# Optimization experiments

Measured on AMD Instinct MI355X. Metric: run time of the kernel, lower is better.

## Reference

```python
import jax, jax.numpy as jnp
import numpy as np

B, T, C, H = 2, 2048, 1024, 16
DH = C // H
EPS = 1e-5


def _rotary(t_len, d_head):
    inv_freq = 1.0 / (10000.0 ** (jnp.arange(0, d_head, 2, dtype=jnp.float32) / d_head))
    t = jnp.arange(t_len, dtype=jnp.float32)
    freqs = t[:, None] * inv_freq[None, :]           # [T, dh/2]
    emb = jnp.concatenate([freqs, freqs], axis=-1)    # [T, dh]
    return jnp.cos(emb), jnp.sin(emb)


def _apply_rope(x, cos, sin):
    # x: [B,H,T,dh]; cos/sin: [T,dh]
    d = x.shape[-1]
    x1, x2 = x[..., : d // 2], x[..., d // 2 :]
    x_rot = jnp.concatenate([-x2, x1], axis=-1)
    return x * cos + x_rot * sin


def _decay_mask(t_len, n_head):
    gammas = 1.0 - 2.0 ** (-5.0 - jnp.arange(n_head, dtype=jnp.float32))  # [H]
    n = jnp.arange(t_len)[:, None]
    m = jnp.arange(t_len)[None, :]
    dist = n - m
    decay = gammas[:, None, None] ** jnp.maximum(dist, 0).astype(jnp.float32)
    return jnp.where(dist[None] >= 0, decay, 0.0)  # [H,T,T]


def setup_inputs() -> dict:
    key = jax.random.key(0)
    ks = jax.random.split(key, 7)
    s = 1.0 / np.sqrt(C)
    return {
        "x": jax.random.normal(ks[0], (B, T, C), dtype=jnp.float32),
        "Wq": jax.random.normal(ks[1], (C, C), dtype=jnp.float32) * s,
        "Wk": jax.random.normal(ks[2], (C, C), dtype=jnp.float32) * s,
        "Wv": jax.random.normal(ks[3], (C, C), dtype=jnp.float32) * s,
        "Wo": jax.random.normal(ks[4], (C, C), dtype=jnp.float32) * s,
        "gn_weight": jnp.ones((C,), dtype=jnp.float32),
        "gn_bias": jnp.zeros((C,), dtype=jnp.float32),
    }


def reference(x, Wq, Wk, Wv, Wo, gn_weight, gn_bias):
    b, t, c = x.shape
    # projections (torch Linear: y = x @ W.T), split heads -> [B,H,T,dh]
    def proj(W):
        return jnp.einsum("btc,oc->bto", x, W).reshape(b, t, H, DH).transpose(0, 2, 1, 3)
    q, k, v = proj(Wq), proj(Wk), proj(Wv)

    cos, sin = _rotary(t, DH)
    q = _apply_rope(q, cos, sin)
    k = _apply_rope(k, cos, sin)

    decay = _decay_mask(t, H)                          # [H,T,T]
    qk = jnp.einsum("bhtd,bhsd->bhts", q, k) * (1.0 / np.sqrt(DH))
    qk = qk * decay[None]
    out = jnp.einsum("bhts,bhsd->bhtd", qk, v)         # [B,H,T,dh]

    # GroupNorm with n_head groups over channels, per token
    out = out.transpose(0, 2, 1, 3)                    # [B,T,H,dh]
    mu = jnp.mean(out, axis=-1, keepdims=True)
    var = jnp.mean((out - mu) ** 2, axis=-1, keepdims=True)
    out = (out - mu) * jax.lax.rsqrt(var + EPS)
    out = out * gn_weight.reshape(H, DH) + gn_bias.reshape(H, DH)

    out = out.reshape(b, t, c)
    return jnp.einsum("btc,oc->bto", out, Wo)
```

## Files before the change

kernel.cpp:

```cpp
#include <hip/hip_runtime.h>
#include <stdint.h>

#define B_ 2
#define T_ 2048
#define C_ 1024
#define H_ 16
#define DH_ 64
#define M_ (B_*T_)

typedef short bhalf8 __attribute__((ext_vector_type(8)));
typedef float floatx4 __attribute__((ext_vector_type(4)));

__device__ __forceinline__ short f2bf(float f) {
  unsigned u = __float_as_uint(f);
  u += 0x7fffu + ((u >> 16) & 1u);
  return (short)(u >> 16);
}

__device__ __forceinline__ void gll16(void* lds_dst, const void* g_src) {
  __builtin_amdgcn_global_load_lds(
      reinterpret_cast<const uint32_t __attribute__((address_space(1)))*>(
          reinterpret_cast<uintptr_t>(g_src)),
      reinterpret_cast<uint32_t __attribute__((address_space(3)))*>(
          reinterpret_cast<uintptr_t>(lds_dst)),
      16, 0, 0);
}

__global__ void cvt_all(
    const float* __restrict__ x,  const float* __restrict__ wq,
    const float* __restrict__ wk, const float* __restrict__ wv,
    const float* __restrict__ wo,
    short* __restrict__ xb, short* __restrict__ wqb, short* __restrict__ wkb,
    short* __restrict__ wvb, short* __restrict__ wob)
{
  int i = blockIdx.x * blockDim.x + threadIdx.x;
  const float* s; short* d; int off;
  if (i < (M_*C_/4)) { s = x; d = xb; off = i; }
  else {
    int j = i - M_*C_/4;
    int w = j >> 18;
    off = j & ((1<<18) - 1);
    s = (w==0) ? wq : (w==1) ? wk : (w==2) ? wv : wo;
    d = (w==0) ? wqb : (w==1) ? wkb : (w==2) ? wvb : wob;
  }
  float4 v = ((const float4*)s)[off];
  short4 o;
  o.x = f2bf(v.x); o.y = f2bf(v.y); o.z = f2bf(v.z); o.w = f2bf(v.w);
  ((short4*)d)[off] = o;
}

__global__ __launch_bounds__(256) void gemm_qkv(
    const short* __restrict__ X,
    const short* __restrict__ Wq, const short* __restrict__ Wk, const short* __restrict__ Wv,
    short* __restrict__ Qb, short* __restrict__ Kb, short* __restrict__ Vt)
{
  __shared__ __align__(16) short As[128*32];
  __shared__ __align__(16) short Bs[128*32];
  const int tid  = threadIdx.x;
  const int lane = tid & 63;
  const int wv   = tid >> 6;
  const int l15  = lane & 15;
  const int quad = lane >> 4;
  const int wm   = (wv >> 1) << 6;
  const int wn   = (wv & 1) << 6;
  const int nx   = blockIdx.x;
  const int m0   = blockIdx.y << 7;
  const int K    = C_;

  const short *Ab, *Bb;
  int nloc, kind;
  if (nx < 8)       { kind = 0; nloc = nx << 7;        Ab = X  + (size_t)m0*K;   Bb = Wq + (size_t)nloc*K; }
  else if (nx < 16) { kind = 1; nloc = (nx - 8) << 7;  Ab = X  + (size_t)m0*K;   Bb = Wk + (size_t)nloc*K; }
  else              { kind = 2; nloc = (nx - 16) << 7; Ab = Wv + (size_t)nloc*K; Bb = X  + (size_t)m0*K;   }

  floatx4 acc[4][4] = {};

  for (int k0 = 0; k0 < K; k0 += 32) {
    __syncthreads();
#pragma unroll
    for (int i = 0; i < 2; ++i) {
      int c = i*256 + tid;
      int row = c >> 2, off = (c & 3) * 8;
      gll16(&As[(i*256 + (wv<<6))*8], Ab + (size_t)row*K + k0 + off);
      gll16(&Bs[(i*256 + (wv<<6))*8], Bb + (size_t)row*K + k0 + off);
    }
    __syncthreads();
    bhalf8 af[4], bfr[4];
#pragma unroll
    for (int rt = 0; rt < 4; ++rt)
      af[rt] = *(const bhalf8*)&As[(wm + rt*16 + l15)*32 + quad*8];
#pragma unroll
    for (int ct = 0; ct < 4; ++ct)
      bfr[ct] = *(const bhalf8*)&Bs[(wn + ct*16 + l15)*32 + quad*8];
#pragma unroll
    for (int rt = 0; rt < 4; ++rt)
#pragma unroll
      for (int ct = 0; ct < 4; ++ct)
        acc[rt][ct] = __builtin_amdgcn_mfma_f32_16x16x32_bf16(af[rt], bfr[ct], acc[rt][ct], 0, 0, 0);
  }

  if (kind < 2) {
    short* Cb = kind ? Kb : Qb;
    const int hh = (nloc + wn) >> 6;
#pragma unroll
    for (int rt = 0; rt < 4; ++rt)
#pragma unroll
      for (int r = 0; r < 4; ++r) {
        int n  = m0 + wm + rt*16 + quad*4 + r;
        int bb = n >> 11, t = n & (T_-1);
        size_t base = ((size_t)(bb*H_ + hh)*T_ + t)*DH_;
        float tf = (float)t;
#pragma unroll
        for (int ct = 0; ct < 2; ++ct) {
          int ii = ct*16 + l15;
          float ang = tf * exp2f((float)ii * (-0.4152410118609203f));
          float sn = __sinf(ang), cs = __cosf(ang);
          float xlo = acc[rt][ct][r], xhi = acc[rt][ct+2][r];
          Cb[base + ii]      = f2bf(xlo*cs - xhi*sn);
          Cb[base + ii + 32] = f2bf(xhi*cs + xlo*sn);
        }
      }
  } else {
#pragma unroll
    for (int rt = 0; rt < 4; ++rt)
#pragma unroll
      for (int r = 0; r < 4; ++r) {
        int o = nloc + wm + rt*16 + quad*4 + r;
#pragma unroll
        for (int ct = 0; ct < 4; ++ct) {
          int n  = m0 + wn + ct*16 + l15;
          int bb = n >> 11, t = n & (T_-1);
          Vt[(size_t)bb*(C_*T_) + (size_t)o*T_ + t] = f2bf(acc[rt][ct][r]);
        }
      }
  }
}

__global__ __launch_bounds__(256) void gemm_out(
    const short* __restrict__ A, const short* __restrict__ Bm, float* __restrict__ Cf)
{
  __shared__ __align__(16) short As[128*64];
  __shared__ __align__(16) short Bs[64*64];
  const int tid = threadIdx.x, lane = tid & 63, wv = tid >> 6;
  const int l15 = lane & 15, quad = lane >> 4;
  const int n0 = blockIdx.x << 6;
  const int m0 = blockIdx.y << 7;

  floatx4 acc[2][4] = {};
  const short* Ab = A  + (size_t)m0 * C_;
  const short* Bb = Bm + (size_t)n0 * C_;

  for (int k0 = 0; k0 < C_; k0 += 64) {
    __syncthreads();
#pragma unroll
    for (int i = 0; i < 4; ++i) {
      int c = (i<<8) + tid, r = c >> 3, g = (c & 7) ^ (r & 7);
      gll16(&As[((i<<8) + (wv<<6))*8], Ab + (size_t)r*C_ + k0 + (g<<3));
    }
#pragma unroll
    for (int i = 0; i < 2; ++i) {
      int c = (i<<8) + tid, r = c >> 3, g = (c & 7) ^ (r & 7);
      gll16(&Bs[((i<<8) + (wv<<6))*8], Bb + (size_t)r*C_ + k0 + (g<<3));
    }
    __syncthreads();
#pragma unroll
    for (int ks = 0; ks < 2; ++ks) {
      bhalf8 af[2], bfr[4];
#pragma unroll
      for (int rt = 0; rt < 2; ++rt) {
        int row = (wv<<5) + rt*16 + l15;
        af[rt] = *(const bhalf8*)&As[(row<<6) + ((((ks<<2)+quad) ^ (row&7))<<3)];
      }
#pragma unroll
      for (int ct = 0; ct < 4; ++ct) {
        int row = ct*16 + l15;
        bfr[ct] = *(const bhalf8*)&Bs[(row<<6) + ((((ks<<2)+quad) ^ (row&7))<<3)];
      }
#pragma unroll
      for (int rt = 0; rt < 2; ++rt)
#pragma unroll
        for (int ct = 0; ct < 4; ++ct)
          acc[rt][ct] = __builtin_amdgcn_mfma_f32_16x16x32_bf16(af[rt], bfr[ct], acc[rt][ct], 0, 0, 0);
    }
  }

#pragma unroll
  for (int rt = 0; rt < 2; ++rt)
#pragma unroll
    for (int r = 0; r < 4; ++r) {
      int n = m0 + (wv<<5) + rt*16 + quad*4 + r;
#pragma unroll
      for (int ct = 0; ct < 4; ++ct)
        Cf[(size_t)n * C_ + n0 + ct*16 + l15] = acc[rt][ct][r];
    }
}

__global__ __launch_bounds__(256, 4) void retention(
    const short* __restrict__ Qb, const short* __restrict__ Kb, const short* __restrict__ Vt,
    const float* __restrict__ gnw, const float* __restrict__ gnb,
    short* __restrict__ Xn)
{
  __shared__ __align__(16) short Ks[2][64*64];
  __shared__ __align__(16) short Vs[2][64*64];
  __shared__ __align__(16) short Ss[64*64];

  const int tid = threadIdx.x, lane = tid & 63, wv = tid >> 6;
  const int l15 = lane & 15, quad = lane >> 4;

  const int flat = blockIdx.x;
  const int bh = (flat & 7) | (((flat >> 8) & 3) << 3);
  const int si = (flat >> 3) & 31;
  const int s  = (si & 1) ? (31 - (si >> 1)) : (si >> 1);
  const int b = bh >> 4, h = bh & 15;
  const int n0 = s << 6;

  const float log2g = log2f(1.f - exp2f(-5.f - (float)h));

  const short* Qg  = Qb + ((size_t)(b*H_ + h)*T_ + n0 + (wv<<4)) * DH_;
  const short* Kg  = Kb + ((size_t)(b*H_ + h)*T_) * DH_;
  const short* Vtg = Vt + (size_t)b*(C_*T_) + (size_t)h*DH_*T_;

  bhalf8 aq[2];
#pragma unroll
  for (int ks = 0; ks < 2; ++ks)
    aq[ks] = *(const bhalf8*)(Qg + (size_t)l15*DH_ + ks*32 + quad*8);

  float rowf[4], colf0[4];
#pragma unroll
  for (int r = 0; r < 4; ++r)
    rowf[r] = exp2f(log2g * (float)((wv<<4) + (quad<<2) + r)) * 0.125f;
#pragma unroll
  for (int ct = 0; ct < 4; ++ct)
    colf0[ct] = exp2f(-log2g * (float)(ct*16 + l15));

  int mt0 = 0;
  while (log2g * (float)(n0 - (mt0 << 6) - 63) < -34.f) ++mt0;
  const int mtmax = s;

  auto stage = [&](int buf, int mt) {
    const int m0s = mt << 6;
#pragma unroll
    for (int i = 0; i < 2; ++i) {
      int slot = (i<<8) + tid;
      int r = slot >> 3, g = (slot & 7) ^ (r & 7);
      gll16(&Ks[buf][((i<<8) + (wv<<6))*8], Kg  + (size_t)(m0s + r)*DH_ + (g<<3));
      gll16(&Vs[buf][((i<<8) + (wv<<6))*8], Vtg + (size_t)r*T_ + m0s + (g<<3));
    }
  };

  floatx4 oacc[4] = {};
  stage(0, mt0);
  int cur = 0;
  for (int mt = mt0; mt <= mtmax; ++mt, cur ^= 1) {
    const int m0 = mt << 6;
    __syncthreads();
    if (mt < mtmax) stage(cur ^ 1, mt + 1);

    floatx4 sacc[4] = {};
#pragma unroll
    for (int ks = 0; ks < 2; ++ks) {
      bhalf8 bk[4];
#pragma unroll
      for (int ct = 0; ct < 4; ++ct) {
        int row = ct*16 + l15;
        bk[ct] = *(const bhalf8*)&Ks[cur][(row<<6) + ((((ks<<2)+quad) ^ (row&7))<<3)];
      }
#pragma unroll
      for (int ct = 0; ct < 4; ++ct)
        sacc[ct] = __builtin_amdgcn_mfma_f32_16x16x32_bf16(aq[ks], bk[ct], sacc[ct], 0, 0, 0);
    }

    const float tilef = exp2f(log2g * (float)(n0 - m0));
    if (mt == mtmax) {
#pragma unroll
      for (int ct = 0; ct < 4; ++ct) {
        float cf = colf0[ct] * tilef;
        int colg = (ct<<1) + (l15>>3);
        int m = m0 + ct*16 + l15;
#pragma unroll
        for (int r = 0; r < 4; ++r) {
          int row = (wv<<4) + (quad<<2) + r;
          float v = (n0 + row >= m) ? sacc[ct][r] * (rowf[r] * cf) : 0.f;
          Ss[(row<<6) + ((colg ^ ((row>>1)&7))<<3) + (l15&7)] = f2bf(v);
        }
      }
    } else {
#pragma unroll
      for (int ct = 0; ct < 4; ++ct) {
        float cf = colf0[ct] * tilef;
        int colg = (ct<<1) + (l15>>3);
#pragma unroll
        for (int r = 0; r < 4; ++r) {
          int row = (wv<<4) + (quad<<2) + r;
          Ss[(row<<6) + ((colg ^ ((row>>1)&7))<<3) + (l15&7)] = f2bf(sacc[ct][r] * (rowf[r] * cf));
        }
      }
    }

#pragma unroll
    for (int ks = 0; ks < 2; ++ks) {
      int row = (wv<<4) + l15;
      bhalf8 as_ = *(const bhalf8*)&Ss[(row<<6) + ((((ks<<2)+quad) ^ ((row>>1)&7))<<3)];
      bhalf8 bv[4];
#pragma unroll
      for (int ct = 0; ct < 4; ++ct) {
        int vrow = ct*16 + l15;
        bv[ct] = *(const bhalf8*)&Vs[cur][(vrow<<6) + ((((ks<<2)+quad) ^ (vrow&7))<<3)];
      }
#pragma unroll
      for (int ct = 0; ct < 4; ++ct)
        oacc[ct] = __builtin_amdgcn_mfma_f32_16x16x32_bf16(as_, bv[ct], oacc[ct], 0, 0, 0);
    }
  }

#pragma unroll
  for (int r = 0; r < 4; ++r) {
    float s1 = oacc[0][r] + oacc[1][r] + oacc[2][r] + oacc[3][r];
    float s2 = oacc[0][r]*oacc[0][r] + oacc[1][r]*oacc[1][r]
             + oacc[2][r]*oacc[2][r] + oacc[3][r]*oacc[3][r];
#pragma unroll
    for (int off = 1; off < 16; off <<= 1) {
      s1 += __shfl_xor(s1, off);
      s2 += __shfl_xor(s2, off);
    }
    float mean = s1 * (1.f/64.f);
    float var  = s2 * (1.f/64.f) - mean*mean;
    float rstd = rsqrtf(var + 1e-5f);
    int t = n0 + (wv<<4) + (quad<<2) + r;
    size_t obase = ((size_t)b*T_ + t)*C_ + h*DH_;
#pragma unroll
    for (int ct = 0; ct < 4; ++ct) {
      int d = ct*16 + l15;
      float y = (oacc[ct][r] - mean)*rstd*gnw[h*DH_ + d] + gnb[h*DH_ + d];
      Xn[obase + d] = f2bf(y);
    }
  }
}

extern "C" void kernel_launch(void* const* d_in, const int* in_sizes, int n_in,
                              void* d_out, int out_size, void* d_ws, size_t ws_size,
                              hipStream_t stream) {
  (void)in_sizes; (void)n_in; (void)out_size; (void)ws_size;
  const float* x   = (const float*)d_in[0];
  const float* Wq  = (const float*)d_in[1];
  const float* Wk  = (const float*)d_in[2];
  const float* Wv  = (const float*)d_in[3];
  const float* Wo  = (const float*)d_in[4];
  const float* gnw = (const float*)d_in[5];
  const float* gnb = (const float*)d_in[6];
  float* out = (float*)d_out;

  char* ws = (char*)d_ws;
  short* Xb  = (short*)(ws);
  short* Wqb = (short*)(ws + (8u<<20));
  short* Wkb = (short*)(ws + (10u<<20));
  short* Wvb = (short*)(ws + (12u<<20));
  short* Wob = (short*)(ws + (14u<<20));
  short* Qb  = (short*)(ws + (16u<<20));
  short* Kb  = (short*)(ws + (24u<<20));
  short* Vtw = (short*)(ws + (32u<<20));
  short* Xn  = (short*)(ws + (40u<<20));

  cvt_all<<<(M_*C_/4 + 4*(C_*C_/4)) / 256, 256, 0, stream>>>(
      x, Wq, Wk, Wv, Wo, Xb, Wqb, Wkb, Wvb, Wob);

  gemm_qkv<<<dim3(24, 32), 256, 0, stream>>>(Xb, Wqb, Wkb, Wvb, Qb, Kb, Vtw);
  retention<<<1024, 256, 0, stream>>>(Qb, Kb, Vtw, gnw, gnb, Xn);
  gemm_out<<<dim3(16, 32), 256, 0, stream>>>(Xn, Wob, out);
}
```

Baseline: 204.4 us.

## Replace quadratic retention with chunkwise recurrent state formulation

Replaces the parallel retention kernel, which loops over all earlier key tiles, with a chunkwise formulation. A transposed K is built, per-segment KV states over groups of 8 chunks are precomputed, and each 64-token chunk combines an intra-chunk quadratic part with the decayed inter-chunk state. The state is stored as split hi/lo bf16 pairs to limit precision loss. This adds two extra kernel launches and aliases workspace buffers that earlier kernels used (Xb, Wqb). It also loops over up to 7 prior chunks inside each block.

```diff
diff --git a/kernel.cpp b/kernel.cpp
--- a/kernel.cpp
+++ b/kernel.cpp
@@ -15,6 +15,9 @@
   unsigned u = __float_as_uint(f);
   u += 0x7fffu + ((u >> 16) & 1u);
   return (short)(u >> 16);
+}
+__device__ __forceinline__ float bf2f(short s) {
+  return __uint_as_float(((unsigned)(unsigned short)s) << 16);
 }
 
 __device__ __forceinline__ void gll16(void* lds_dst, const void* g_src) {
@@ -195,30 +198,130 @@
     }
 }
 
-__global__ __launch_bounds__(256, 4) void retention(
-    const short* __restrict__ Qb, const short* __restrict__ Kb, const short* __restrict__ Vt,
+__global__ __launch_bounds__(256) void transpose_k(
+    const short* __restrict__ Kb, short* __restrict__ Kt)
+{
+  __shared__ short tile[64*66];
+  const int idx = blockIdx.x, bh = idx >> 5, tc = idx & 31;
+  const int t0 = tc << 6;
+  const short* src = Kb + ((size_t)bh*T_ + t0) * DH_;
+  int row = threadIdx.x >> 2, c0 = (threadIdx.x & 3) << 4;
+  *(int4*)&tile[row*66 + c0]     = *(const int4*)&src[row*64 + c0];
+  *(int4*)&tile[row*66 + c0 + 8] = *(const int4*)&src[row*64 + c0 + 8];
+  __syncthreads();
+  short* dst = Kt + (size_t)bh*DH_*T_;
+  int d = threadIdx.x >> 2, k0 = (threadIdx.x & 3) << 4;
+  short tmp[16];
+#pragma unroll
+  for (int i = 0; i < 16; ++i) tmp[i] = tile[(k0 + i)*66 + d];
+  *(int4*)&dst[(size_t)d*T_ + t0 + k0]     = *(const int4*)&tmp[0];
+  *(int4*)&dst[(size_t)d*T_ + t0 + k0 + 8] = *(const int4*)&tmp[8];
+}
+
+__global__ __launch_bounds__(256) void seg_state(
+    const short* __restrict__ Kt, const short* __restrict__ Vt,
+    short* __restrict__ Pseg)
+{
+  __shared__ __align__(16) short Ks[64*64];
+  __shared__ __align__(16) short Vs[64*64];
+  const int tid = threadIdx.x, lane = tid & 63, wv = tid >> 6;
+  const int l15 = lane & 15, quad = lane >> 4;
+  const int wrow = wv << 4;
+  const int bh = blockIdx.x >> 2, p = blockIdx.x & 3;
+  const int h = bh & 15;
+  const float log2g = log2f(1.f - exp2f(-5.f - (float)h));
+  const float g64 = exp2f(log2g * 64.f);
+
+  float wgt[16];
+#pragma unroll
+  for (int ks = 0; ks < 2; ++ks)
+#pragma unroll
+    for (int i = 0; i < 8; ++i)
+      wgt[ks*8 + i] = exp2f(log2g * (float)(64 - (ks*32 + (quad<<3) + i)));
+
+  const short* Ktg = Kt + (size_t)bh*DH_*T_;
+  const short* Vtg = Vt + (size_t)bh*DH_*T_;
+
+  floatx4 acc[4] = {};
+  for (int j = 0; j < 8; ++j) {
+    const int m0 = ((p<<3) + j) << 6;
+    __syncthreads();
+#pragma unroll
+    for (int i = 0; i < 2; ++i) {
+      int slot = (i<<8) + tid;
+      int r = slot >> 3, g = (slot & 7) ^ (r & 7);
+      gll16(&Ks[((i<<8) + (wv<<6))*8], Ktg + (size_t)r*T_ + m0 + (g<<3));
+      gll16(&Vs[((i<<8) + (wv<<6))*8], Vtg + (size_t)r*T_ + m0 + (g<<3));
+    }
+    __syncthreads();
+#pragma unroll
+    for (int ct = 0; ct < 4; ++ct)
+#pragma unroll
+      for (int r = 0; r < 4; ++r) acc[ct][r] *= g64;
+#pragma unroll
+    for (int ks = 0; ks < 2; ++ks) {
+      int row = wrow + l15;
+      bhalf8 va = *(const bhalf8*)&Vs[(row<<6) + ((((ks<<2)+quad) ^ (row&7))<<3)];
+      bhalf8 aw;
+#pragma unroll
+      for (int i = 0; i < 8; ++i) aw[i] = f2bf(bf2f(va[i]) * wgt[ks*8 + i]);
+      bhalf8 bk[4];
+#pragma unroll
+      for (int ct = 0; ct < 4; ++ct) {
+        int kr = ct*16 + l15;
+        bk[ct] = *(const bhalf8*)&Ks[(kr<<6) + ((((ks<<2)+quad) ^ (kr&7))<<3)];
+      }
+#pragma unroll
+      for (int ct = 0; ct < 4; ++ct)
+        acc[ct] = __builtin_amdgcn_mfma_f32_16x16x32_bf16(aw, bk[ct], acc[ct], 0, 0, 0);
+    }
+  }
+  size_t base = (size_t)(bh*4 + p) * 2 * 4096;
+#pragma unroll
+  for (int ct = 0; ct < 4; ++ct)
+#pragma unroll
+    for (int r = 0; r < 4; ++r) {
+      int e = wrow + (quad<<2) + r, d = ct*16 + l15;
+      float x = acc[ct][r];
+      short hi = f2bf(x);
+      short lo = f2bf(x - bf2f(hi));
+      Pseg[base + e*64 + d]        = hi;
+      Pseg[base + 4096 + e*64 + d] = lo;
+    }
+}
+
+__global__ __launch_bounds__(256) void retention_chunk(
+    const short* __restrict__ Qb, const short* __restrict__ Kb,
+    const short* __restrict__ Kt, const short* __restrict__ Vt,
+    const short* __restrict__ Pseg,
     const float* __restrict__ gnw, const float* __restrict__ gnb,
     short* __restrict__ Xn)
 {
-  __shared__ __align__(16) short Ks[2][64*64];
-  __shared__ __align__(16) short Vs[2][64*64];
-  __shared__ __align__(16) short Ss[64*64];
+  __shared__ __align__(16) short Vs[64*64];
+  __shared__ __align__(16) short Kts[64*64];
+  __shared__ __align__(16) short KSs[64*64];
+  __shared__ __align__(16) short Sh[64*64];
+  __shared__ __align__(16) short Sl[64*64];
 
   const int tid = threadIdx.x, lane = tid & 63, wv = tid >> 6;
   const int l15 = lane & 15, quad = lane >> 4;
-
-  const int flat = blockIdx.x;
-  const int bh = (flat & 7) | (((flat >> 8) & 3) << 3);
-  const int si = (flat >> 3) & 31;
-  const int s  = (si & 1) ? (31 - (si >> 1)) : (si >> 1);
+  const int wrow = wv << 4;
+
+  const int idx = blockIdx.x;
+  const int bh = idx & 31;
+  const int cc = idx >> 5;
+  const int c  = ((cc & 7) << 2) | (cc >> 3);
+  const int p = c >> 3, j = c & 7;
   const int b = bh >> 4, h = bh & 15;
-  const int n0 = s << 6;
+  const int n0 = c << 6;
 
   const float log2g = log2f(1.f - exp2f(-5.f - (float)h));
-
-  const short* Qg  = Qb + ((size_t)(b*H_ + h)*T_ + n0 + (wv<<4)) * DH_;
-  const short* Kg  = Kb + ((size_t)(b*H_ + h)*T_) * DH_;
-  const short* Vtg = Vt + (size_t)b*(C_*T_) + (size_t)h*DH_*T_;
+  const float g64 = exp2f(log2g * 64.f);
+
+  const short* Qg  = Qb + ((size_t)bh*T_ + n0 + wrow) * DH_;
+  const short* Kg  = Kb + (size_t)bh*T_*DH_;
+  const short* Ktg = Kt + (size_t)bh*DH_*T_;
+  const short* Vtg = Vt + (size_t)bh*DH_*T_;
 
   bhalf8 aq[2];
 #pragma unroll
@@ -228,89 +331,158 @@
   float rowf[4], colf0[4];
 #pragma unroll
   for (int r = 0; r < 4; ++r)
-    rowf[r] = exp2f(log2g * (float)((wv<<4) + (quad<<2) + r)) * 0.125f;
+    rowf[r] = exp2f(log2g * (float)(wrow + (quad<<2) + r)) * 0.125f;
 #pragma unroll
   for (int ct = 0; ct < 4; ++ct)
     colf0[ct] = exp2f(-log2g * (float)(ct*16 + l15));
 
-  int mt0 = 0;
-  while (log2g * (float)(n0 - (mt0 << 6) - 63) < -34.f) ++mt0;
-  const int mtmax = s;
-
-  auto stage = [&](int buf, int mt) {
-    const int m0s = mt << 6;
-#pragma unroll
-    for (int i = 0; i < 2; ++i) {
-      int slot = (i<<8) + tid;
-      int r = slot >> 3, g = (slot & 7) ^ (r & 7);
-      gll16(&Ks[buf][((i<<8) + (wv<<6))*8], Kg  + (size_t)(m0s + r)*DH_ + (g<<3));
-      gll16(&Vs[buf][((i<<8) + (wv<<6))*8], Vtg + (size_t)r*T_ + m0s + (g<<3));
-    }
-  };
-
+  const bool has_state = (c > 0);
+
+  floatx4 st[4] = {};
+  if (j > 0) {
+    float wgt[16];
+#pragma unroll
+    for (int ks = 0; ks < 2; ++ks)
+#pragma unroll
+      for (int i = 0; i < 8; ++i)
+        wgt[ks*8 + i] = exp2f(log2g * (float)(64 - (ks*32 + (quad<<3) + i)));
+    for (int jp = 0; jp < j; ++jp) {
+      if (log2g * (float)((j - 1 - jp) << 6) < -34.f) continue;
+      const int m0 = ((p<<3) + jp) << 6;
+      __syncthreads();
+#pragma unroll
+      for (int i = 0; i < 2; ++i) {
+        int slot = (i<<8) + tid;
+        int r = slot >> 3, g = (slot & 7) ^ (r & 7);
+        gll16(&Kts[((i<<8) + (wv<<6))*8], Ktg + (size_t)r*T_ + m0 + (g<<3));
+        gll16(&Vs[((i<<8) + (wv<<6))*8],  Vtg + (size_t)r*T_ + m0 + (g<<3));
+      }
+      __syncthreads();
+#pragma unroll
+      for (int ct = 0; ct < 4; ++ct)
+#pragma unroll
+        for (int r = 0; r < 4; ++r) st[ct][r] *= g64;
+#pragma unroll
+      for (int ks = 0; ks < 2; ++ks) {
+        int row = wrow + l15;
+        bhalf8 va = *(const bhalf8*)&Vs[(row<<6) + ((((ks<<2)+quad) ^ (row&7))<<3)];
+        bhalf8 aw;
+#pragma unroll
+        for (int i = 0; i < 8; ++i) aw[i] = f2bf(bf2f(va[i]) * wgt[ks*8 + i]);
+        bhalf8 bk[4];
+#pragma unroll
+        for (int ct = 0; ct < 4; ++ct) {
+          int kr = ct*16 + l15;
+          bk[ct] = *(const bhalf8*)&Kts[(kr<<6) + ((((ks<<2)+quad) ^ (kr&7))<<3)];
+        }
+#pragma unroll
+        for (int ct = 0; ct < 4; ++ct)
+          st[ct] = __builtin_amdgcn_mfma_f32_16x16x32_bf16(aw, bk[ct], st[ct], 0, 0, 0);
+      }
+    }
+  }
+  for (int pp = 0; pp < p; ++pp) {
+    float wexp = log2g * (float)(n0 - ((pp + 1) << 9));
+    if (wexp < -34.f) continue;
+    float w = exp2f(wexp);
+    const short* Pg = Pseg + (size_t)(bh*4 + pp) * 2 * 4096;
+#pragma unroll
+    for (int ct = 0; ct < 4; ++ct)
+#pragma unroll
+      for (int r = 0; r < 4; ++r) {
+        int e = wrow + (quad<<2) + r, d = ct*16 + l15;
+        st[ct][r] += w * (bf2f(Pg[e*64 + d]) + bf2f(Pg[4096 + e*64 + d]));
+      }
+  }
+  if (has_state) {
+#pragma unroll
+    for (int ct = 0; ct < 4; ++ct)
+#pragma unroll
+      for (int r = 0; r < 4; ++r) {
+        int e = wrow + (quad<<2) + r, d = ct*16 + l15;
+        float x = st[ct][r];
+        short hi = f2bf(x);
+        short lo = f2bf(x - bf2f(hi));
+        int addr = (e<<6) + ((((d>>3) ^ (e&7))<<3)) + (d&7);
+        Sh[addr] = hi; Sl[addr] = lo;
+      }
+  }
+
+  __syncthreads();
+#pragma unroll
+  for (int i = 0; i < 2; ++i) {
+    int slot = (i<<8) + tid;
+    int r = slot >> 3, g = (slot & 7) ^ (r & 7);
+    gll16(&KSs[((i<<8) + (wv<<6))*8], Kg  + (size_t)(n0 + r)*DH_ + (g<<3));
+    gll16(&Vs[((i<<8) + (wv<<6))*8],  Vtg + (size_t)r*T_ + n0 + (g<<3));
+  }
+  __syncthreads();
+
+  floatx4 sacc[4] = {};
+#pragma unroll
+  for (int ks = 0; ks < 2; ++ks) {
+    bhalf8 bk[4];
+#pragma unroll
+    for (int ct = 0; ct < 4; ++ct) {
+      int row = ct*16 + l15;
+      bk[ct] = *(const bhalf8*)&KSs[(row<<6) + ((((ks<<2)+quad) ^ (row&7))<<3)];
+    }
+#pragma unroll
+    for (int ct = 0; ct < 4; ++ct)
+      sacc[ct] = __builtin_amdgcn_mfma_f32_16x16x32_bf16(aq[ks], bk[ct], sacc[ct], 0, 0, 0);
+  }
+  __syncthreads();
+#pragma unroll
+  for (int ct = 0; ct < 4; ++ct) {
+    float cf = colf0[ct];
+    int colg = (ct<<1) + (l15>>3);
+    int m = ct*16 + l15;
+#pragma unroll
+    for (int r = 0; r < 4; ++r) {
+      int row = wrow + (quad<<2) + r;
+      float v = (row >= m) ? sacc[ct][r] * (rowf[r] * cf) : 0.f;
+      KSs[(row<<6) + ((colg ^ ((row>>1)&7))<<3) + (l15&7)] = f2bf(v);
+    }
+  }
   floatx4 oacc[4] = {};
-  stage(0, mt0);
-  int cur = 0;
-  for (int mt = mt0; mt <= mtmax; ++mt, cur ^= 1) {
-    const int m0 = mt << 6;
-    __syncthreads();
-    if (mt < mtmax) stage(cur ^ 1, mt + 1);
-
-    floatx4 sacc[4] = {};
+#pragma unroll
+  for (int ks = 0; ks < 2; ++ks) {
+    int row = wrow + l15;
+    bhalf8 as_ = *(const bhalf8*)&KSs[(row<<6) + ((((ks<<2)+quad) ^ ((row>>1)&7))<<3)];
+    bhalf8 bv[4];
+#pragma unroll
+    for (int ct = 0; ct < 4; ++ct) {
+      int vrow = ct*16 + l15;
+      bv[ct] = *(const bhalf8*)&Vs[(vrow<<6) + ((((ks<<2)+quad) ^ (vrow&7))<<3)];
+    }
+#pragma unroll
+    for (int ct = 0; ct < 4; ++ct)
+      oacc[ct] = __builtin_amdgcn_mfma_f32_16x16x32_bf16(as_, bv[ct], oacc[ct], 0, 0, 0);
+  }
+
+  if (has_state) {
+    floatx4 iacc[4] = {};
 #pragma unroll
     for (int ks = 0; ks < 2; ++ks) {
-      bhalf8 bk[4];
+      bhalf8 bhf[4], blf[4];
 #pragma unroll
       for (int ct = 0; ct < 4; ++ct) {
-        int row = ct*16 + l15;
-        bk[ct] = *(const bhalf8*)&Ks[cur][(row<<6) + ((((ks<<2)+quad) ^ (row&7))<<3)];
-      }
-#pragma unroll
-      for (int ct = 0; ct < 4; ++ct)
-        sacc[ct] = __builtin_amdgcn_mfma_f32_16x16x32_bf16(aq[ks], bk[ct], sacc[ct], 0, 0, 0);
-    }
-
-    const float tilef = exp2f(log2g * (float)(n0 - m0));
-    if (mt == mtmax) {
+        int er = ct*16 + l15;
+        int ga = ((((ks<<2)+quad) ^ (er&7))<<3);
+        bhf[ct] = *(const bhalf8*)&Sh[(er<<6) + ga];
+        blf[ct] = *(const bhalf8*)&Sl[(er<<6) + ga];
+      }
 #pragma unroll
       for (int ct = 0; ct < 4; ++ct) {
-        float cf = colf0[ct] * tilef;
-        int colg = (ct<<1) + (l15>>3);
-        int m = m0 + ct*16 + l15;
-#pragma unroll
-        for (int r = 0; r < 4; ++r) {
-          int row = (wv<<4) + (quad<<2) + r;
-          float v = (n0 + row >= m) ? sacc[ct][r] * (rowf[r] * cf) : 0.f;
-          Ss[(row<<6) + ((colg ^ ((row>>1)&7))<<3) + (l15&7)] = f2bf(v);
-        }
-      }
-    } else {
-#pragma unroll
-      for (int ct = 0; ct < 4; ++ct) {
-        float cf = colf0[ct] * tilef;
-        int colg = (ct<<1) + (l15>>3);
-#pragma unroll
-        for (int r = 0; r < 4; ++r) {
-          int row = (wv<<4) + (quad<<2) + r;
-          Ss[(row<<6) + ((colg ^ ((row>>1)&7))<<3) + (l15&7)] = f2bf(sacc[ct][r] * (rowf[r] * cf));
-        }
-      }
-    }
-
-#pragma unroll
-    for (int ks = 0; ks < 2; ++ks) {
-      int row = (wv<<4) + l15;
-      bhalf8 as_ = *(const bhalf8*)&Ss[(row<<6) + ((((ks<<2)+quad) ^ ((row>>1)&7))<<3)];
-      bhalf8 bv[4];
-#pragma unroll
-      for (int ct = 0; ct < 4; ++ct) {
-        int vrow = ct*16 + l15;
-        bv[ct] = *(const bhalf8*)&Vs[cur][(vrow<<6) + ((((ks<<2)+quad) ^ (vrow&7))<<3)];
-      }
-#pragma unroll
-      for (int ct = 0; ct < 4; ++ct)
-        oacc[ct] = __builtin_amdgcn_mfma_f32_16x16x32_bf16(as_, bv[ct], oacc[ct], 0, 0, 0);
-    }
+        iacc[ct] = __builtin_amdgcn_mfma_f32_16x16x32_bf16(aq[ks], bhf[ct], iacc[ct], 0, 0, 0);
+        iacc[ct] = __builtin_amdgcn_mfma_f32_16x16x32_bf16(aq[ks], blf[ct], iacc[ct], 0, 0, 0);
+      }
+    }
+#pragma unroll
+    for (int ct = 0; ct < 4; ++ct)
+#pragma unroll
+      for (int r = 0; r < 4; ++r)
+        oacc[ct][r] += rowf[r] * iacc[ct][r];
   }
 
 #pragma unroll
@@ -326,7 +498,7 @@
     float mean = s1 * (1.f/64.f);
     float var  = s2 * (1.f/64.f) - mean*mean;
     float rstd = rsqrtf(var + 1e-5f);
-    int t = n0 + (wv<<4) + (quad<<2) + r;
+    int t = n0 + wrow + (quad<<2) + r;
     size_t obase = ((size_t)b*T_ + t)*C_ + h*DH_;
 #pragma unroll
     for (int ct = 0; ct < 4; ++ct) {
@@ -351,20 +523,24 @@
   float* out = (float*)d_out;
 
   char* ws = (char*)d_ws;
-  short* Xb  = (short*)(ws);
-  short* Wqb = (short*)(ws + (8u<<20));
-  short* Wkb = (short*)(ws + (10u<<20));
-  short* Wvb = (short*)(ws + (12u<<20));
-  short* Wob = (short*)(ws + (14u<<20));
-  short* Qb  = (short*)(ws + (16u<<20));
-  short* Kb  = (short*)(ws + (24u<<20));
-  short* Vtw = (short*)(ws + (32u<<20));
-  short* Xn  = (short*)(ws + (40u<<20));
+  short* Xb   = (short*)(ws);
+  short* Ktb  = (short*)(ws);
+  short* Wqb  = (short*)(ws + (8u<<20));
+  short* Pseg = (short*)(ws + (8u<<20));
+  short* Wkb  = (short*)(ws + (10u<<20));
+  short* Wvb  = (short*)(ws + (12u<<20));
+  short* Wob  = (short*)(ws + (14u<<20));
+  short* Qb   = (short*)(ws + (16u<<20));
+  short* Kb   = (short*)(ws + (24u<<20));
+  short* Vtw  = (short*)(ws + (32u<<20));
+  short* Xn   = (short*)(ws + (40u<<20));
 
   cvt_all<<<(M_*C_/4 + 4*(C_*C_/4)) / 256, 256, 0, stream>>>(
       x, Wq, Wk, Wv, Wo, Xb, Wqb, Wkb, Wvb, Wob);
 
   gemm_qkv<<<dim3(24, 32), 256, 0, stream>>>(Xb, Wqb, Wkb, Wvb, Qb, Kb, Vtw);
-  retention<<<1024, 256, 0, stream>>>(Qb, Kb, Vtw, gnw, gnb, Xn);
+  transpose_k<<<1024, 256, 0, stream>>>(Kb, Ktb);
+  seg_state<<<128, 256, 0, stream>>>(Ktb, Vtw, Pseg);
+  retention_chunk<<<1024, 256, 0, stream>>>(Qb, Kb, Ktb, Vtw, Pseg, gnw, gnb, Xn);
   gemm_out<<<dim3(16, 32), 256, 0, stream>>>(Xn, Wob, out);
 }
```

New measurement: 187.6 us. -8.2%, faster.
